# Optimization experiments

Measured on AMD Instinct MI355X. Metric: run time of the kernel, lower is better.

## Reference

```python
import jax, jax.numpy as jnp
import numpy as np

N_NODES = 50000
N_EDGES = 600000
N_COMM = 500
COMM_EDGES = 8000
NFEAT = 128
NHID = 128
NCLASS = 10
NLAYERS = 3
NHEADS = 8
EPS = 1e-5


def setup_inputs() -> dict:
    key = jax.random.key(0)
    ks = jax.random.split(key, 32)
    s = 0.05
    def rn(i, shape, scale=s):
        return (jax.random.normal(ks[i], shape, dtype=jnp.float32) * scale)
    return {
        "node_features": jax.random.normal(ks[0], (N_NODES, NFEAT), dtype=jnp.float32),
        "node_edge_index": jax.random.randint(ks[1], (2, N_EDGES), 0, N_NODES),
        "comm_features": jax.random.normal(ks[2], (N_COMM, NHID), dtype=jnp.float32),
        "comm_edge_index": jax.random.randint(ks[3], (2, COMM_EDGES), 0, N_COMM),
        "node_to_comm_map": jax.random.randint(ks[4], (N_NODES,), 0, N_COMM),
        # node-branch GCN params (nfeat == nhid so weights stack)
        "node_W": rn(5, (NLAYERS, NHID, NHID)),
        "node_b": rn(6, (NLAYERS, NHID)),
        "node_bn_g": 1.0 + rn(7, (NLAYERS, NHID)),
        "node_bn_b": rn(8, (NLAYERS, NHID)),
        # community-branch GCN params
        "comm_W": rn(9, (NLAYERS, NHID, NHID)),
        "comm_b": rn(10, (NLAYERS, NHID)),
        "comm_bn_g": 1.0 + rn(11, (NLAYERS, NHID)),
        "comm_bn_b": rn(12, (NLAYERS, NHID)),
        # MultiheadAttention params (torch layout: y = x @ W.T + b)
        "attn_in_w": rn(13, (3 * NHID, NHID)),
        "attn_in_b": rn(14, (3 * NHID,)),
        "attn_out_w": rn(15, (NHID, NHID)),
        "attn_out_b": rn(16, (NHID,)),
        # gate LayerNorm
        "ln_g": 1.0 + rn(17, (NHID,)),
        "ln_b": rn(18, (NHID,)),
        # classifier: Linear(128,64) -> BN -> ReLU -> Linear(64,10)
        "cls_W1": rn(19, (NHID, NHID // 2)),
        "cls_b1": rn(20, (NHID // 2,)),
        "cls_bn_g": 1.0 + rn(21, (NHID // 2,)),
        "cls_bn_b": rn(22, (NHID // 2,)),
        "cls_W2": rn(23, (NHID // 2, NCLASS)),
        "cls_b2": rn(24, (NCLASS,)),
    }


def _gcn_norm(edge_index, n):
    # PyG gcn_norm: add self-loops, symmetric D^-1/2 (A+I) D^-1/2
    loop = jnp.arange(n)
    src = jnp.concatenate([edge_index[0], loop])
    dst = jnp.concatenate([edge_index[1], loop])
    deg = jax.ops.segment_sum(jnp.ones(src.shape[0], jnp.float32), dst, num_segments=n)
    dinv = jnp.where(deg > 0, deg ** -0.5, 0.0)
    return src, dst, dinv[src] * dinv[dst]


def _gcn_stack(x, edge_index, Ws, bs, gs, betas):
    n = x.shape[0]
    src, dst, norm = _gcn_norm(edge_index, n)
    h = x
    for i in range(Ws.shape[0]):
        h_prev = h
        m = h @ Ws[i]  # linear commutes with normalized aggregation
        agg = jax.ops.segment_sum(m[src] * norm[:, None], dst, num_segments=n) + bs[i]
        mu = agg.mean(0)
        var = agg.var(0)  # biased, as torch BN training
        hb = (agg - mu) / jnp.sqrt(var + EPS) * gs[i] + betas[i]
        h = jax.nn.relu(hb)
        if i > 0:
            h = h + h_prev
    return h


def _mha(x, wi, bi, wo, bo):
    # x: [N, S=2, E]
    N, S, E = x.shape
    dh = E // NHEADS
    qkv = x @ wi.T + bi
    q, k, v = jnp.split(qkv, 3, axis=-1)
    q = q.reshape(N, S, NHEADS, dh)
    k = k.reshape(N, S, NHEADS, dh)
    v = v.reshape(N, S, NHEADS, dh)
    att = jnp.einsum('nqhd,nkhd->nhqk', q, k) / np.float32(np.sqrt(dh))
    att = jax.nn.softmax(att, axis=-1)
    o = jnp.einsum('nhqk,nkhd->nqhd', att, v).reshape(N, S, E)
    return o @ wo.T + bo


def reference(node_features, node_edge_index, comm_features, comm_edge_index,
              node_to_comm_map, node_W, node_b, node_bn_g, node_bn_b,
              comm_W, comm_b, comm_bn_g, comm_bn_b,
              attn_in_w, attn_in_b, attn_out_w, attn_out_b,
              ln_g, ln_b, cls_W1, cls_b1, cls_bn_g, cls_bn_b, cls_W2, cls_b2):
    h_node = _gcn_stack(node_features, node_edge_index, node_W, node_b, node_bn_g, node_bn_b)
    h_comm = _gcn_stack(comm_features, comm_edge_index, comm_W, comm_b, comm_bn_g, comm_bn_b)
    safe = jnp.clip(node_to_comm_map, 0, h_comm.shape[0] - 1)
    h_comm_exp = h_comm[safe]  # [N, nhid] cross-scale gather
    comb = jnp.stack([h_node, h_comm_exp], axis=1)  # [N, 2, nhid]
    attended = _mha(comb, attn_in_w, attn_in_b, attn_out_w, attn_out_b)
    x = attended.mean(axis=1) + h_node
    mu = x.mean(-1, keepdims=True)
    var = x.var(-1, keepdims=True)
    h_final = (x - mu) / jnp.sqrt(var + EPS) * ln_g + ln_b
    z = h_final @ cls_W1 + cls_b1
    zm = z.mean(0)
    zv = z.var(0)
    z = jax.nn.relu((z - zm) / jnp.sqrt(zv + EPS) * cls_bn_g + cls_bn_b)
    logits = z @ cls_W2 + cls_b2
    return jax.nn.log_softmax(logits, axis=-1)
```

## Files before the change

kernel.cpp:

```cpp
#include <hip/hip_runtime.h>
#include <hip/hip_bf16.h>
#include <cstdint>
#include <cstddef>


typedef __attribute__((ext_vector_type(8))) short bf16x8;
typedef __attribute__((ext_vector_type(4))) float f32x4;

#define EPSV 1e-5f

__device__ __forceinline__ float b2f(unsigned short u) {
    union { unsigned int i; float f; } x; x.i = ((unsigned int)u) << 16; return x.f;
}
__device__ __forceinline__ unsigned short f2b(float f) {
    union { float f; unsigned int i; } x; x.f = f;
    unsigned int i = x.i;
    return (unsigned short)((i + 0x7fffu + ((i >> 16) & 1u)) >> 16);
}

__global__ void prep_kernel(const float* __restrict__ node_W, const float* __restrict__ comm_W,
                            const float* __restrict__ cls_W1, const float* __restrict__ attn_in_w,
                            const float* __restrict__ attn_out_w, const float* __restrict__ comm_feat,
                            const float* __restrict__ node_feat,
                            unsigned short* __restrict__ WtN, unsigned short* __restrict__ WtC,
                            unsigned short* __restrict__ W1t, unsigned short* __restrict__ WinB,
                            unsigned short* __restrict__ WoutB, unsigned short* __restrict__ cfb,
                            unsigned short* __restrict__ nfb, int nC128, int nN128,
                            const int* __restrict__ ndst, int* __restrict__ cnt_n, int nE,
                            const int* __restrict__ cdst, int* __restrict__ cnt_c, int cE) {
    int idx = blockIdx.x * 256 + threadIdx.x;
    if (idx < 49152) {
        int l = idx >> 14, e = idx & 16383;
        int j = e & 7, lane = (e >> 3) & 63, kc = (e >> 9) & 3, t = e >> 11;
        int col = t * 16 + (lane & 15);
        int k = (lane >> 4) * 8 + kc * 32 + j;
        WtN[idx] = f2b(node_W[l * 16384 + k * 128 + col]); return;
    }
    idx -= 49152;
    if (idx < 49152) {
        int l = idx >> 14, e = idx & 16383;
        int j = e & 7, lane = (e >> 3) & 63, kc = (e >> 9) & 3, t = e >> 11;
        int col = t * 16 + (lane & 15);
        int k = (lane >> 4) * 8 + kc * 32 + j;
        WtC[idx] = f2b(comm_W[l * 16384 + k * 128 + col]); return;
    }
    idx -= 49152;
    if (idx < 8192) {
        int e = idx;
        int j = e & 7, lane = (e >> 3) & 63, kc = (e >> 9) & 3, t = e >> 11;
        int col = t * 16 + (lane & 15);
        int k = (lane >> 4) * 8 + kc * 32 + j;
        W1t[idx] = f2b(cls_W1[k * 64 + col]); return;
    }
    idx -= 8192;
    if (idx < 49152) {
        int e = idx;
        int j = e & 7, lane = (e >> 3) & 63, kc = (e >> 9) & 3, t = e >> 11;
        int col = t * 16 + (lane & 15);
        int k = (lane >> 4) * 8 + kc * 32 + j;
        WinB[idx] = f2b(attn_in_w[col * 128 + k]); return;
    }
    idx -= 49152;
    if (idx < 16384) {
        int e = idx;
        int j = e & 7, lane = (e >> 3) & 63, kc = (e >> 9) & 3, t = e >> 11;
        int col = t * 16 + (lane & 15);
        int k = (lane >> 4) * 8 + kc * 32 + j;
        WoutB[idx] = f2b(attn_out_w[col * 128 + k]); return;
    }
    idx -= 16384;
    if (idx < nC128) { cfb[idx] = f2b(comm_feat[idx]); return; }
    idx -= nC128;
    if (idx < nN128) { nfb[idx] = f2b(node_feat[idx]); return; }
    idx -= nN128;
    long eg = (long)idx * 4;
    if (eg < (long)nE + cE) {
        int dd[4]; int wh[4];
#pragma unroll
        for (int k = 0; k < 4; ++k) {
            long e = eg + k;
            if (e < nE) { dd[k] = ndst[e]; wh[k] = 0; }
            else if (e - nE < cE) { dd[k] = cdst[e - nE]; wh[k] = 1; }
            else wh[k] = -1;
        }
#pragma unroll
        for (int k = 0; k < 4; ++k) {
            if (wh[k] == 0) atomicAdd(&cnt_n[dd[k]], 1);
            else if (wh[k] == 1) atomicAdd(&cnt_c[dd[k]], 1);
        }
    }
}

__global__ void scan_block_dual(const int* __restrict__ cnt_n, int* __restrict__ rs_n,
                                int* __restrict__ bsum_n, int nN, int nbN,
                                const int* __restrict__ cnt_c, int* __restrict__ rs_c,
                                int* __restrict__ bsum_c, int nC,
                                float* __restrict__ di_n, float* __restrict__ di_c) {
    __shared__ int tmp[2048];
    int nbC = (nC + 1023) >> 10;
    int extra = (int)blockIdx.x - (nbN + nbC);
    if (extra >= 0) {
        int g = extra * 1024 + (int)threadIdx.x;
        if (g < nN) di_n[g] = rsqrtf((float)cnt_n[g] + 1.0f);
        else { int gc = g - nN; if (gc < nC) di_c[gc] = rsqrtf((float)cnt_c[gc] + 1.0f); }
        return;
    }
    const int* cnt; int* excl; int* bsum; int n, lb;
    if ((int)blockIdx.x < nbN) { cnt = cnt_n; excl = rs_n; bsum = bsum_n; n = nN; lb = blockIdx.x; }
    else { cnt = cnt_c; excl = rs_c; bsum = bsum_c; n = nC; lb = blockIdx.x - nbN; }
    int tid = threadIdx.x;
    int gid = lb * 1024 + tid;
    int v = (gid < n) ? ((cnt[gid] + 7) & ~7) : 0;
    int buf = 0;
    tmp[tid] = v;
    __syncthreads();
    for (int d = 1; d < 1024; d <<= 1) {
        int t = tmp[buf * 1024 + tid];
        int add = (tid >= d) ? tmp[buf * 1024 + tid - d] : 0;
        tmp[(1 - buf) * 1024 + tid] = t + add;
        buf = 1 - buf;
        __syncthreads();
    }
    int inc = tmp[buf * 1024 + tid];
    if (gid < n) excl[gid] = inc - v;
    if (tid == 1023) bsum[lb] = inc;
}

__global__ void scan_add_dual(int* __restrict__ rs_n, const int* __restrict__ bsum_n,
                              int* __restrict__ cur_n, int nN,
                              int* __restrict__ rs_c, const int* __restrict__ bsum_c,
                              int* __restrict__ cur_c, int nC) {
    int gid = blockIdx.x * 256 + threadIdx.x;
    if (gid < nN) {
        int lb = gid >> 10;
        int p = 0;
        for (int i = 0; i < lb; ++i) p += bsum_n[i];
        int v = rs_n[gid] + p;
        rs_n[gid] = v; cur_n[gid] = v;
    } else {
        int g = gid - nN;
        if (g < nC) {
            int lb = g >> 10;
            int p = 0;
            for (int i = 0; i < lb; ++i) p += bsum_c[i];
            int v = rs_c[g] + p;
            rs_c[g] = v; cur_c[g] = v;
        }
    }
}

__device__ __forceinline__ void gemm_wave_128(const unsigned short* __restrict__ A,
                                              const unsigned short* __restrict__ Bt,
                                              const float* __restrict__ di,
                                              unsigned short* __restrict__ D,
                                              int M, int m0, int lane) {
    int r = lane & 15, q = lane >> 4;
    int arow = m0 + r; if (arow >= M) arow = M - 1;
    const unsigned short* ap = A + (size_t)arow * 128 + q * 8;
    bf16x8 afrag[4];
#pragma unroll
    for (int kc = 0; kc < 4; ++kc)
        afrag[kc] = *(const bf16x8*)(const void*)(ap + kc * 32);
    float dsc[4];
#pragma unroll
    for (int t = 0; t < 4; ++t) {
        int row = m0 + q * 4 + t; if (row >= M) row = M - 1;
        dsc[t] = di[row];
    }
#pragma unroll
    for (int tt = 0; tt < 8; ++tt) {
        f32x4 acc = {0.f, 0.f, 0.f, 0.f};
#pragma unroll
        for (int kc = 0; kc < 4; ++kc) {
            bf16x8 bfrag = *(const bf16x8*)(const void*)(Bt + (((size_t)tt * 4 + kc) << 9) + lane * 8);
            acc = __builtin_amdgcn_mfma_f32_16x16x32_bf16(afrag[kc], bfrag, acc, 0, 0, 0);
        }
        int n0 = tt * 16;
#pragma unroll
        for (int t = 0; t < 4; ++t) {
            int row = m0 + q * 4 + t;
            if (row < M) D[(size_t)row * 128 + n0 + r] = f2b(acc[t] * dsc[t]);
        }
    }
}

__global__ __launch_bounds__(256) void gemm_fill_kernel(
    const unsigned short* __restrict__ A0, const unsigned short* __restrict__ Bt0,
    const float* __restrict__ di0, unsigned short* __restrict__ D0, int M0, int blocksA,
    const unsigned short* __restrict__ A1, const unsigned short* __restrict__ Bt1,
    const float* __restrict__ di1, unsigned short* __restrict__ D1, int M1, int blocksB,
    const int* __restrict__ ns, const int* __restrict__ ndst,
    int* __restrict__ cur_n, unsigned short* __restrict__ csrc_n, int nE,
    const int* __restrict__ cs, const int* __restrict__ cdst,
    int* __restrict__ cur_c, unsigned short* __restrict__ csrc_c, int cE) {
    int blk = blockIdx.x;
    if (blk < blocksA + blocksB) {
        const unsigned short *A, *Bt; const float* di; unsigned short* D; int M, lb;
        if (blk < blocksA) { A = A0; Bt = Bt0; di = di0; D = D0; M = M0; lb = blk; }
        else { A = A1; Bt = Bt1; di = di1; D = D1; M = M1; lb = blk - blocksA; }
        int m0 = (lb * 4 + (int)(threadIdx.x >> 6)) * 16;
        if (m0 >= M) return;
        gemm_wave_128(A, Bt, di, D, M, m0, threadIdx.x & 63);
        return;
    }
    long eg = ((long)(blk - blocksA - blocksB) * 256 + threadIdx.x) * 4;
    if (eg >= (long)nE + cE) return;
    int ss[4], pos[4], wh[4];
#pragma unroll
    for (int k = 0; k < 4; ++k) {
        long e = eg + k;
        if (e < nE) {
            ss[k] = ns[e]; int d = ndst[e];
            pos[k] = atomicAdd(&cur_n[d], 1); wh[k] = 0;
        } else if (e - nE < cE) {
            long ee = e - nE;
            ss[k] = cs[ee]; int d = cdst[ee];
            pos[k] = atomicAdd(&cur_c[d], 1); wh[k] = 1;
        } else wh[k] = -1;
    }
#pragma unroll
    for (int k = 0; k < 4; ++k) {
        if (wh[k] == 0)
            __builtin_nontemporal_store((unsigned short)(ss[k] + 1), csrc_n + pos[k]);
        else if (wh[k] == 1)
            __builtin_nontemporal_store((unsigned short)(ss[k] + 1), csrc_c + pos[k]);
    }
}

__global__ __launch_bounds__(256) void gather_dual(
    const unsigned short* __restrict__ m0, const int* __restrict__ rs0,
    const int* __restrict__ cnt0, const unsigned short* __restrict__ cs0,
    const float* __restrict__ di0, const float* __restrict__ b0,
    float* __restrict__ agg0, float* __restrict__ bins0, int n0, int blocksA,
    const unsigned short* __restrict__ m1, const int* __restrict__ rs1,
    const int* __restrict__ cnt1, const unsigned short* __restrict__ cs1,
    const float* __restrict__ di1, const float* __restrict__ b1,
    float* __restrict__ agg1, float* __restrict__ bins1, int n1) {
    __shared__ float lsum[4][128], lsq[4][128];
    int blk = blockIdx.x;
    const unsigned short* m; const int *rs, *cnt; const unsigned short* cs;
    const float *di, *bias;
    float *agg, *bins; int n, lb;
    if (blk < blocksA) { m = m0; rs = rs0; cnt = cnt0; cs = cs0; di = di0; bias = b0; agg = agg0; bins = bins0; n = n0; lb = blk; }
    else { m = m1; rs = rs1; cnt = cnt1; cs = cs1; di = di1; bias = b1; agg = agg1; bins = bins1; n = n1; lb = blk - blocksA; }
    int wib = threadIdx.x >> 6, lane = threadIdx.x & 63;
    int node = lb * 4 + wib;
    bool act = node < n;
    float a0 = 0.f, a1 = 0.f;
    if (act) {
        int start = rs[node];
        int end = start + ((cnt[node] + 7) & ~7);
        for (int i = start; i < end; i += 8) {
            int s[8]; unsigned int v[8];
#pragma unroll
            for (int j = 0; j < 8; ++j) s[j] = cs[i + j];
#pragma unroll
            for (int j = 0; j < 8; ++j) {
                int si = s[j] ? s[j] - 1 : node;
                v[j] = *(const unsigned int*)(m + (size_t)si * 128 + 2 * lane);
            }
#pragma unroll
            for (int j = 0; j < 8; ++j) {
                float wj = s[j] ? 1.f : 0.f;
                a0 += b2f((unsigned short)(v[j] & 0xffff)) * wj;
                a1 += b2f((unsigned short)(v[j] >> 16)) * wj;
            }
        }
        unsigned int v = *(const unsigned int*)(m + (size_t)node * 128 + 2 * lane);
        a0 += b2f((unsigned short)(v & 0xffff));
        a1 += b2f((unsigned short)(v >> 16));
        float d = di[node];
        a0 = a0 * d + bias[2 * lane];
        a1 = a1 * d + bias[2 * lane + 1];
        float2 o; o.x = a0; o.y = a1;
        ((float2*)(agg + (size_t)node * 128))[lane] = o;
    }
    lsum[wib][2 * lane] = a0;       lsum[wib][2 * lane + 1] = a1;
    lsq[wib][2 * lane] = a0 * a0;   lsq[wib][2 * lane + 1] = a1 * a1;
    __syncthreads();
    int t = threadIdx.x;
    int bb = (lb & 31) * 256;
    if (t < 128) {
        float v = lsum[0][t] + lsum[1][t] + lsum[2][t] + lsum[3][t];
        atomicAdd(&bins[bb + t], v);
    } else {
        int c = t - 128;
        float v = lsq[0][c] + lsq[1][c] + lsq[2][c] + lsq[3][c];
        atomicAdd(&bins[bb + 128 + c], v);
    }
}

__global__ __launch_bounds__(256) void applygemm_dual(
    const float* __restrict__ agg0, const float* __restrict__ bins0,
    const float* __restrict__ g0, const float* __restrict__ be0,
    unsigned short* __restrict__ hb0, const unsigned short* __restrict__ Bt0,
    const float* __restrict__ di0, unsigned short* __restrict__ D0,
    int n0, int blocksA, int useRes,
    const float* __restrict__ agg1, const float* __restrict__ bins1,
    const float* __restrict__ g1, const float* __restrict__ be1,
    unsigned short* __restrict__ hb1, const unsigned short* __restrict__ Bt1,
    const float* __restrict__ di1, unsigned short* __restrict__ D1, int n1) {
    __shared__ float sc[128], sh[128], bs[256];
    __shared__ unsigned short hrow_s[64 * 136];
    int blk = blockIdx.x;
    const float *agg, *bins, *g, *be, *di; unsigned short *hb, *D;
    const unsigned short* Bt; int n, lb;
    if (blk < blocksA) { agg = agg0; bins = bins0; g = g0; be = be0; hb = hb0; Bt = Bt0; di = di0; D = D0; n = n0; lb = blk; }
    else { agg = agg1; bins = bins1; g = g1; be = be1; hb = hb1; Bt = Bt1; di = di1; D = D1; n = n1; lb = blk - blocksA; }
    int t = threadIdx.x;
    {
        float a = 0.f;
#pragma unroll
        for (int b = 0; b < 32; ++b) a += bins[b * 256 + t];
        bs[t] = a;
    }
    __syncthreads();
    if (t < 128) {
        float inv = 1.f / (float)n;
        float mean = bs[t] * inv;
        float var = bs[128 + t] * inv - mean * mean;
        float rstd = rsqrtf(var + EPSV);
        float s = g[t] * rstd;
        sc[t] = s;
        sh[t] = be[t] - mean * s;
    }
    __syncthreads();
    int row0 = lb * 64;
#pragma unroll
    for (int it = 0; it < 8; ++it) {
        int base = row0 * 128 + it * 1024 + t * 4;
        if (base < n * 128) {
            float4 a = *(const float4*)(agg + base);
            ushort4 h = *(const ushort4*)(hb + base);
            int f = base & 127;
            float v0 = fmaxf(a.x * sc[f] + sh[f], 0.f);
            float v1 = fmaxf(a.y * sc[f + 1] + sh[f + 1], 0.f);
            float v2 = fmaxf(a.z * sc[f + 2] + sh[f + 2], 0.f);
            float v3 = fmaxf(a.w * sc[f + 3] + sh[f + 3], 0.f);
            if (useRes) { v0 += b2f(h.x); v1 += b2f(h.y); v2 += b2f(h.z); v3 += b2f(h.w); }
            ushort4 o; o.x = f2b(v0); o.y = f2b(v1); o.z = f2b(v2); o.w = f2b(v3);
            *(ushort4*)(hb + base) = o;
            int lr = (base >> 7) - row0;
            *(ushort4*)(hrow_s + lr * 136 + f) = o;
        }
    }
    __syncthreads();
    int lane = t & 63, w = t >> 6;
    int m0 = row0 + w * 16;
    if (m0 >= n) return;
    int r = lane & 15, q = lane >> 4;
    int arow = m0 + r; if (arow >= n) arow = n - 1;
    const unsigned short* ap = hrow_s + (arow - row0) * 136 + q * 8;
    bf16x8 afrag[4];
#pragma unroll
    for (int kc = 0; kc < 4; ++kc)
        afrag[kc] = *(const bf16x8*)(const void*)(ap + kc * 32);
    float dsc[4];
#pragma unroll
    for (int t4 = 0; t4 < 4; ++t4) {
        int row = m0 + q * 4 + t4; if (row >= n) row = n - 1;
        dsc[t4] = di[row];
    }
#pragma unroll
    for (int tt = 0; tt < 8; ++tt) {
        f32x4 acc = {0.f, 0.f, 0.f, 0.f};
#pragma unroll
        for (int kc = 0; kc < 4; ++kc) {
            bf16x8 bfrag = *(const bf16x8*)(const void*)(Bt + (((size_t)tt * 4 + kc) << 9) + lane * 8);
            acc = __builtin_amdgcn_mfma_f32_16x16x32_bf16(afrag[kc], bfrag, acc, 0, 0, 0);
        }
        int n0c = tt * 16;
#pragma unroll
        for (int t4 = 0; t4 < 4; ++t4) {
            int row = m0 + q * 4 + t4;
            if (row < n) D[(size_t)row * 128 + n0c + r] = f2b(acc[t4] * dsc[t4]);
        }
    }
}

__global__ __launch_bounds__(256) void apply_dual(
    const float* __restrict__ agg0, const float* __restrict__ bins0,
    const float* __restrict__ g0, const float* __restrict__ be0,
    unsigned short* __restrict__ hb0, int n0, int blocksA, int useRes,
    const float* __restrict__ agg1, const float* __restrict__ bins1,
    const float* __restrict__ g1, const float* __restrict__ be1,
    unsigned short* __restrict__ hb1, int n1,
    int doCq, const unsigned short* __restrict__ WinB,
    const float* __restrict__ binb, float* __restrict__ cqkv) {
    __shared__ float sc[128], sh[128], bs[256];
    __shared__ unsigned short crow_s[32 * 136];
    int blk = blockIdx.x;
    bool isComm = blk >= blocksA;
    const float *agg, *bins, *g, *be; unsigned short* hb; int n, lb;
    if (!isComm) { agg = agg0; bins = bins0; g = g0; be = be0; hb = hb0; n = n0; lb = blk; }
    else { agg = agg1; bins = bins1; g = g1; be = be1; hb = hb1; n = n1; lb = blk - blocksA; }
    int t = threadIdx.x;
    {
        float a = 0.f;
#pragma unroll
        for (int b = 0; b < 32; ++b) a += bins[b * 256 + t];
        bs[t] = a;
    }
    __syncthreads();
    if (t < 128) {
        float inv = 1.f / (float)n;
        float mean = bs[t] * inv;
        float var = bs[128 + t] * inv - mean * mean;
        float rstd = rsqrtf(var + EPSV);
        float s = g[t] * rstd;
        sc[t] = s;
        sh[t] = be[t] - mean * s;
    }
    __syncthreads();
    bool stage = doCq && isComm;
#pragma unroll
    for (int it = 0; it < 4; ++it) {
        int base = (lb * 4 + it) * 1024 + t * 4;
        if (base < n * 128) {
            float4 a = *(const float4*)(agg + base);
            ushort4 h = *(const ushort4*)(hb + base);
            int f = base & 127;
            float v0 = fmaxf(a.x * sc[f] + sh[f], 0.f);
            float v1 = fmaxf(a.y * sc[f + 1] + sh[f + 1], 0.f);
            float v2 = fmaxf(a.z * sc[f + 2] + sh[f + 2], 0.f);
            float v3 = fmaxf(a.w * sc[f + 3] + sh[f + 3], 0.f);
            if (useRes) { v0 += b2f(h.x); v1 += b2f(h.y); v2 += b2f(h.z); v3 += b2f(h.w); }
            ushort4 o; o.x = f2b(v0); o.y = f2b(v1); o.z = f2b(v2); o.w = f2b(v3);
            *(ushort4*)(hb + base) = o;
            if (stage) {
                int row = (base >> 7) - lb * 32;
                *(ushort4*)(crow_s + row * 136 + (base & 127)) = o;
            }
        }
    }
    if (stage) {
        __syncthreads();
        int lane = t & 63, w = t >> 6;
        int r = lane & 15, q = lane >> 4;
        int rg = w & 1;
        const unsigned short* ap = crow_s + (rg * 16 + r) * 136 + q * 8;
        bf16x8 afrag[4];
#pragma unroll
        for (int kc = 0; kc < 4; ++kc)
            afrag[kc] = *(const bf16x8*)(const void*)(ap + kc * 32);
        int t0 = (w >> 1) * 12;
        for (int tt = t0; tt < t0 + 12; ++tt) {
            f32x4 acc = {0.f, 0.f, 0.f, 0.f};
#pragma unroll
            for (int kc = 0; kc < 4; ++kc) {
                bf16x8 bfrag = *(const bf16x8*)(const void*)(WinB + (((size_t)tt * 4 + kc) << 9) + lane * 8);
                acc = __builtin_amdgcn_mfma_f32_16x16x32_bf16(afrag[kc], bfrag, acc, 0, 0, 0);
            }
            int n0c = tt * 16;
            float bv = binb[n0c + r];
#pragma unroll
            for (int t4 = 0; t4 < 4; ++t4) {
                int row = lb * 32 + rg * 16 + q * 4 + t4;
                if (row < n) cqkv[(size_t)row * 384 + n0c + r] = acc[t4] + bv;
            }
        }
    }
}

__global__ __launch_bounds__(256) void mha_fused_kernel(
    const unsigned short* __restrict__ hbn, const int* __restrict__ map,
    const float* __restrict__ cqkv,
    const unsigned short* __restrict__ WinB, const float* __restrict__ bin,
    const unsigned short* __restrict__ WoutB, const float* __restrict__ bout,
    const float* __restrict__ lng, const float* __restrict__ lnb,
    const unsigned short* __restrict__ W1t, const float* __restrict__ b1v,
    float* __restrict__ z, float* __restrict__ zbins, int nN, int nC) {
    __shared__ unsigned short obf_s[16 * 136];
    __shared__ float att_s[16 * 132];

    int b = blockIdx.x;
    int hg = threadIdx.x >> 6;
    int lane = threadIdx.x & 63;
    int r = lane & 15, q = lane >> 4;

    int arow = b * 16 + r; if (arow >= nN) arow = nN - 1;
    const unsigned short* ap = hbn + (size_t)arow * 128 + q * 8;
    bf16x8 afrag[4];
#pragma unroll
    for (int kc = 0; kc < 4; ++kc)
        afrag[kc] = *(const bf16x8*)(const void*)(ap + kc * 32);

    const float* cp[4];
#pragma unroll
    for (int t = 0; t < 4; ++t) {
        int nt = b * 16 + q * 4 + t; if (nt >= nN) nt = nN - 1;
        int c = map[nt]; c = c < 0 ? 0 : (c >= nC ? nC - 1 : c);
        cp[t] = cqkv + (size_t)c * 384;
    }

#pragma unroll
    for (int c = 0; c < 2; ++c) {
        int h = hg * 2 + c;
        f32x4 qa, ka, va;
#pragma unroll
        for (int p = 0; p < 3; ++p) {
            int tt = p * 8 + h;
            f32x4 acc = {0.f, 0.f, 0.f, 0.f};
#pragma unroll
            for (int kc = 0; kc < 4; ++kc) {
                bf16x8 bfrag = *(const bf16x8*)(const void*)(WinB + (((size_t)tt * 4 + kc) << 9) + lane * 8);
                acc = __builtin_amdgcn_mfma_f32_16x16x32_bf16(afrag[kc], bfrag, acc, 0, 0, 0);
            }
            float bv = bin[tt * 16 + r];
#pragma unroll
            for (int t = 0; t < 4; ++t) acc[t] += bv;
            if (p == 0) qa = acc; else if (p == 1) ka = acc; else va = acc;
        }
        float qc[4], kc_[4], vc[4];
#pragma unroll
        for (int t = 0; t < 4; ++t) {
            const float* cpt = cp[t] + h * 16 + r;
            qc[t] = cpt[0]; kc_[t] = cpt[128]; vc[t] = cpt[256];
        }
#pragma unroll
        for (int t = 0; t < 4; ++t) {
            float s00 = qa[t] * ka[t];
            float s01 = qa[t] * kc_[t];
            float s10 = qc[t] * ka[t];
            float s11 = qc[t] * kc_[t];
#pragma unroll
            for (int mku = 1; mku <= 8; mku <<= 1) {
                s00 += __shfl_xor(s00, mku); s01 += __shfl_xor(s01, mku);
                s10 += __shfl_xor(s10, mku); s11 += __shfl_xor(s11, mku);
            }
            s00 *= 0.25f; s01 *= 0.25f; s10 *= 0.25f; s11 *= 0.25f;
            float m0 = fmaxf(s00, s01), m1 = fmaxf(s10, s11);
            float e00 = __expf(s00 - m0), e01 = __expf(s01 - m0);
            float e10 = __expf(s10 - m1), e11 = __expf(s11 - m1);
            float i0 = 1.f / (e00 + e01), i1 = 1.f / (e10 + e11);
            float o0 = (e00 * va[t] + e01 * vc[t]) * i0;
            float o1 = (e10 * va[t] + e11 * vc[t]) * i1;
            obf_s[(q * 4 + t) * 136 + h * 16 + r] = f2b(0.5f * (o0 + o1));
        }
    }
    __syncthreads();

    bf16x8 ofrag[4];
#pragma unroll
    for (int kc = 0; kc < 4; ++kc)
        ofrag[kc] = *(const bf16x8*)(const void*)(obf_s + r * 136 + q * 8 + kc * 32);
#pragma unroll
    for (int c = 0; c < 2; ++c) {
        int tt = hg * 2 + c;
        f32x4 acc = {0.f, 0.f, 0.f, 0.f};
#pragma unroll
        for (int kc = 0; kc < 4; ++kc) {
            bf16x8 bfrag = *(const bf16x8*)(const void*)(WoutB + (((size_t)tt * 4 + kc) << 9) + lane * 8);
            acc = __builtin_amdgcn_mfma_f32_16x16x32_bf16(ofrag[kc], bfrag, acc, 0, 0, 0);
        }
        int n0 = tt * 16;
        float bv = bout[n0 + r];
#pragma unroll
        for (int t = 0; t < 4; ++t)
            att_s[(q * 4 + t) * 132 + n0 + r] = acc[t] + bv;
    }
    __syncthreads();
    unsigned short* hf_s = obf_s;

    {
        int nl = threadIdx.x >> 4;
        int j = threadIdx.x & 15;
        int gnode = b * 16 + nl;
        if (gnode >= nN) gnode = nN - 1;
        const unsigned short* hrow = hbn + (size_t)gnode * 128 + j * 8;
        ushort4 ha = *(const ushort4*)(hrow);
        ushort4 hbv = *(const ushort4*)(hrow + 4);
        float x[8]; float s = 0.f, s2 = 0.f;
        x[0] = att_s[nl * 132 + j * 8 + 0] + b2f(ha.x);
        x[1] = att_s[nl * 132 + j * 8 + 1] + b2f(ha.y);
        x[2] = att_s[nl * 132 + j * 8 + 2] + b2f(ha.z);
        x[3] = att_s[nl * 132 + j * 8 + 3] + b2f(ha.w);
        x[4] = att_s[nl * 132 + j * 8 + 4] + b2f(hbv.x);
        x[5] = att_s[nl * 132 + j * 8 + 5] + b2f(hbv.y);
        x[6] = att_s[nl * 132 + j * 8 + 6] + b2f(hbv.z);
        x[7] = att_s[nl * 132 + j * 8 + 7] + b2f(hbv.w);
#pragma unroll
        for (int i = 0; i < 8; ++i) { s += x[i]; s2 += x[i] * x[i]; }
        s += __shfl_xor(s, 1);  s2 += __shfl_xor(s2, 1);
        s += __shfl_xor(s, 2);  s2 += __shfl_xor(s2, 2);
        s += __shfl_xor(s, 4);  s2 += __shfl_xor(s2, 4);
        s += __shfl_xor(s, 8);  s2 += __shfl_xor(s2, 8);
        float mu = s * (1.f / 128.f);
        float var = s2 * (1.f / 128.f) - mu * mu;
        float rstd = rsqrtf(var + EPSV);
        ushort4 o1, o2;
        o1.x = f2b((x[0] - mu) * rstd * lng[j * 8 + 0] + lnb[j * 8 + 0]);
        o1.y = f2b((x[1] - mu) * rstd * lng[j * 8 + 1] + lnb[j * 8 + 1]);
        o1.z = f2b((x[2] - mu) * rstd * lng[j * 8 + 2] + lnb[j * 8 + 2]);
        o1.w = f2b((x[3] - mu) * rstd * lng[j * 8 + 3] + lnb[j * 8 + 3]);
        o2.x = f2b((x[4] - mu) * rstd * lng[j * 8 + 4] + lnb[j * 8 + 4]);
        o2.y = f2b((x[5] - mu) * rstd * lng[j * 8 + 5] + lnb[j * 8 + 5]);
        o2.z = f2b((x[6] - mu) * rstd * lng[j * 8 + 6] + lnb[j * 8 + 6]);
        o2.w = f2b((x[7] - mu) * rstd * lng[j * 8 + 7] + lnb[j * 8 + 7]);
        *(ushort4*)(hf_s + nl * 136 + j * 8) = o1;
        *(ushort4*)(hf_s + nl * 136 + j * 8 + 4) = o2;
    }
    __syncthreads();

    {
        bf16x8 hfrag[4];
#pragma unroll
        for (int kc = 0; kc < 4; ++kc)
            hfrag[kc] = *(const bf16x8*)(const void*)(hf_s + r * 136 + q * 8 + kc * 32);
        f32x4 acc = {0.f, 0.f, 0.f, 0.f};
#pragma unroll
        for (int kc = 0; kc < 4; ++kc) {
            bf16x8 bfrag = *(const bf16x8*)(const void*)(W1t + (((size_t)hg * 4 + kc) << 9) + lane * 8);
            acc = __builtin_amdgcn_mfma_f32_16x16x32_bf16(hfrag[kc], bfrag, acc, 0, 0, 0);
        }
        float bv = b1v[hg * 16 + r];
        float s = 0.f, s2 = 0.f;
#pragma unroll
        for (int t = 0; t < 4; ++t) {
            int row = b * 16 + q * 4 + t;
            if (row < nN) {
                float v = acc[t] + bv;
                z[(size_t)row * 64 + hg * 16 + r] = v;
                s += v; s2 += v * v;
            }
        }
        s += __shfl_xor(s, 16);  s2 += __shfl_xor(s2, 16);
        s += __shfl_xor(s, 32);  s2 += __shfl_xor(s2, 32);
        if (lane < 16) {
            int bb = (b & 31) * 128;
            atomicAdd(&zbins[bb + hg * 16 + r], s);
            atomicAdd(&zbins[bb + 64 + hg * 16 + r], s2);
        }
    }
}

__global__ __launch_bounds__(256) void final_kernel(const float* __restrict__ z,
                                                    const float* __restrict__ zbins,
                                                    const float* __restrict__ g,
                                                    const float* __restrict__ be,
                                                    const float* __restrict__ W2,
                                                    const float* __restrict__ b2v,
                                                    float* __restrict__ out, int nN) {
    __shared__ float zs[128];
    int t = threadIdx.x;
    if (t < 128) {
        float a = 0.f;
#pragma unroll
        for (int b = 0; b < 32; ++b) a += zbins[b * 128 + t];
        zs[t] = a;
    }
    __syncthreads();
    int lane = t & 63;
    float inv = 1.f / (float)nN;
    float mean = zs[lane] * inv;
    float var = zs[64 + lane] * inv - mean * mean;
    float sc = g[lane] * rsqrtf(var + EPSV);
    float sh = be[lane] - mean * sc;
    const float* wrow = W2 + lane * 10;
#pragma unroll
    for (int it = 0; it < 4; ++it) {
        int node = blockIdx.x * 16 + (t >> 6) * 4 + it;
        float v = 0.f;
        if (node < nN) v = fmaxf(z[(size_t)node * 64 + lane] * sc + sh, 0.f);
        float p[10];
#pragma unroll
        for (int c = 0; c < 10; ++c) p[c] = v * wrow[c];
#pragma unroll
        for (int off = 32; off >= 1; off >>= 1) {
#pragma unroll
            for (int c = 0; c < 10; ++c) p[c] += __shfl_xor(p[c], off);
        }
        if (node < nN) {
            float l[10], mx = -1e30f;
#pragma unroll
            for (int c = 0; c < 10; ++c) { l[c] = p[c] + b2v[c]; mx = fmaxf(mx, l[c]); }
            float se = 0.f;
#pragma unroll
            for (int c = 0; c < 10; ++c) se += expf(l[c] - mx);
            float lse = mx + logf(se);
            if (lane < 10) out[(size_t)node * 10 + lane] = l[lane] - lse;
        }
    }
}

static inline int cdiv(long a, long b) { return (int)((a + b - 1) / b); }

extern "C" void kernel_launch(void* const* d_in, const int* in_sizes, int n_in,
                              void* d_out, int out_size, void* d_ws, size_t ws_size,
                              hipStream_t stream) {
    const float* node_feat = (const float*)d_in[0];
    const int*   nedge     = (const int*)d_in[1];
    const float* comm_feat = (const float*)d_in[2];
    const int*   cedge     = (const int*)d_in[3];
    const int*   n2c       = (const int*)d_in[4];
    const float* node_W    = (const float*)d_in[5];
    const float* node_b    = (const float*)d_in[6];
    const float* node_g    = (const float*)d_in[7];
    const float* node_beta = (const float*)d_in[8];
    const float* comm_W    = (const float*)d_in[9];
    const float* comm_b    = (const float*)d_in[10];
    const float* comm_g    = (const float*)d_in[11];
    const float* comm_beta = (const float*)d_in[12];
    const float* attn_in_w = (const float*)d_in[13];
    const float* attn_in_b = (const float*)d_in[14];
    const float* attn_out_w= (const float*)d_in[15];
    const float* attn_out_b= (const float*)d_in[16];
    const float* ln_g      = (const float*)d_in[17];
    const float* ln_b      = (const float*)d_in[18];
    const float* cls_W1    = (const float*)d_in[19];
    const float* cls_b1    = (const float*)d_in[20];
    const float* cls_bn_g  = (const float*)d_in[21];
    const float* cls_bn_b  = (const float*)d_in[22];
    const float* cls_W2    = (const float*)d_in[23];
    const float* cls_b2    = (const float*)d_in[24];

    const int nN = in_sizes[0] / 128;
    const int nE = in_sizes[1] / 2;
    const int nC = in_sizes[2] / 128;
    const int cE = in_sizes[3] / 2;
    const int padE_n = nE + 8 * nN;
    const int padE_c = cE + 8 * nC;

    char* ws = (char*)d_ws;
    size_t off = 0;
    auto alloc = [&](size_t bytes) -> char* {
        char* p = ws + off;
        off = (off + bytes + 255) & ~(size_t)255;
        return p;
    };
    size_t zero_begin = off;
    int*   cnt_n  = (int*)alloc((size_t)nN * 4);
    int*   cur_n  = (int*)alloc((size_t)nN * 4);
    int*   cnt_c  = (int*)alloc((size_t)nC * 4);
    int*   cur_c  = (int*)alloc((size_t)nC * 4);
    float* bins_n = (float*)alloc((size_t)3 * 32 * 256 * 4);
    float* bins_c = (float*)alloc((size_t)3 * 32 * 256 * 4);
    float* zbins  = (float*)alloc((size_t)32 * 128 * 4);
    unsigned short* csrc_n = (unsigned short*)alloc((size_t)padE_n * 2);
    unsigned short* csrc_c = (unsigned short*)alloc((size_t)padE_c * 2);
    size_t zero_bytes = off - zero_begin;
    int*   rs_n   = (int*)alloc((size_t)(nN + 1) * 4);
    int*   bsum_n = (int*)alloc(256 * 4);
    float* dinv_n = (float*)alloc((size_t)nN * 4);
    int*   rs_c   = (int*)alloc((size_t)(nC + 1) * 4);
    int*   bsum_c = (int*)alloc(256 * 4);
    float* dinv_c = (float*)alloc((size_t)nC * 4);
    unsigned short* hb_n  = (unsigned short*)alloc((size_t)nN * 256);
    unsigned short* hb_c  = (unsigned short*)alloc((size_t)nC * 256);
    unsigned short* cfb   = (unsigned short*)alloc((size_t)nC * 256);
    unsigned short* m_cb  = (unsigned short*)alloc((size_t)nC * 256);
    float*          agg_c = (float*)alloc((size_t)nC * 512);
    float*          cqkv  = (float*)alloc((size_t)nC * 384 * 4);
    unsigned short* WtN  = (unsigned short*)alloc((size_t)3 * 16384 * 2);
    unsigned short* WtC  = (unsigned short*)alloc((size_t)3 * 16384 * 2);
    unsigned short* W1t  = (unsigned short*)alloc((size_t)64 * 128 * 2);
    unsigned short* WinB = (unsigned short*)alloc((size_t)384 * 128 * 2);
    unsigned short* WoutB= (unsigned short*)alloc((size_t)128 * 128 * 2);
    unsigned short* m_nb = (unsigned short*)alloc((size_t)nN * 256);
    float*          agg_n= (float*)alloc((size_t)nN * 512);
    unsigned short* nfb  = (unsigned short*)agg_n;
    float*          z    = agg_n;

    hipMemsetAsync(ws + zero_begin, 0, zero_bytes, stream);

    long prepN = 49152L * 3 + 8192 + 16384 + (long)nC * 128 + (long)nN * 128;
    long cntThreads = ((long)nE + cE + 3) / 4;
    long prepTotal = prepN + cntThreads;
    prep_kernel<<<cdiv(prepTotal, 256), 256, 0, stream>>>(
        node_W, comm_W, cls_W1, attn_in_w, attn_out_w, comm_feat, node_feat,
        WtN, WtC, W1t, WinB, WoutB, cfb, nfb, nC * 128, nN * 128,
        nedge + nE, cnt_n, nE, cedge + cE, cnt_c, cE);

    int nbN = cdiv(nN, 1024), nbC = cdiv(nC, 1024);
    int dinvB = cdiv((long)nN + nC, 1024);
    scan_block_dual<<<nbN + nbC + dinvB, 1024, 0, stream>>>(
        cnt_n, rs_n, bsum_n, nN, nbN, cnt_c, rs_c, bsum_c, nC, dinv_n, dinv_c);
    scan_add_dual<<<cdiv((long)nN + nC, 256), 256, 0, stream>>>(
        rs_n, bsum_n, cur_n, nN, rs_c, bsum_c, cur_c, nC);

    int gemmA = cdiv(nN, 64), gemmB = cdiv(nC, 64);
    int fillB = cdiv((long)nE + cE, 1024);
    int gatA = cdiv(nN, 4), gatB = cdiv(nC, 4);
    int appA = cdiv((long)nN * 128, 4096), appB = cdiv((long)nC * 128, 4096);

    gemm_fill_kernel<<<gemmA + gemmB + fillB, 256, 0, stream>>>(
        nfb, WtN, dinv_n, m_nb, nN, gemmA,
        cfb, WtC, dinv_c, m_cb, nC, gemmB,
        nedge, nedge + nE, cur_n, csrc_n, nE,
        cedge, cedge + cE, cur_c, csrc_c, cE);
    gather_dual<<<gatA + gatB, 256, 0, stream>>>(
        m_nb, rs_n, cnt_n, csrc_n, dinv_n, node_b, agg_n, bins_n, nN, gatA,
        m_cb, rs_c, cnt_c, csrc_c, dinv_c, comm_b, agg_c, bins_c, nC);
    applygemm_dual<<<gemmA + gemmB, 256, 0, stream>>>(
        agg_n, bins_n, node_g, node_beta, hb_n, WtN + 16384, dinv_n, m_nb, nN, gemmA, 0,
        agg_c, bins_c, comm_g, comm_beta, hb_c, WtC + 16384, dinv_c, m_cb, nC);
    gather_dual<<<gatA + gatB, 256, 0, stream>>>(
        m_nb, rs_n, cnt_n, csrc_n, dinv_n, node_b + 128, agg_n, bins_n + 32 * 256, nN, gatA,
        m_cb, rs_c, cnt_c, csrc_c, dinv_c, comm_b + 128, agg_c, bins_c + 32 * 256, nC);
    applygemm_dual<<<gemmA + gemmB, 256, 0, stream>>>(
        agg_n, bins_n + 32 * 256, node_g + 128, node_beta + 128, hb_n, WtN + 2 * 16384, dinv_n, m_nb, nN, gemmA, 1,
        agg_c, bins_c + 32 * 256, comm_g + 128, comm_beta + 128, hb_c, WtC + 2 * 16384, dinv_c, m_cb, nC);
    gather_dual<<<gatA + gatB, 256, 0, stream>>>(
        m_nb, rs_n, cnt_n, csrc_n, dinv_n, node_b + 256, agg_n, bins_n + 2 * 32 * 256, nN, gatA,
        m_cb, rs_c, cnt_c, csrc_c, dinv_c, comm_b + 256, agg_c, bins_c + 2 * 32 * 256, nC);
    apply_dual<<<appA + appB, 256, 0, stream>>>(
        agg_n, bins_n + 2 * 32 * 256, node_g + 256, node_beta + 256, hb_n, nN, appA, 1,
        agg_c, bins_c + 2 * 32 * 256, comm_g + 256, comm_beta + 256, hb_c, nC,
        1, WinB, attn_in_b, cqkv);

    mha_fused_kernel<<<cdiv(nN, 16), 256, 0, stream>>>(
        hb_n, n2c, cqkv, WinB, attn_in_b, WoutB, attn_out_b, ln_g, ln_b,
        W1t, cls_b1, z, zbins, nN, nC);

    final_kernel<<<cdiv(nN, 16), 256, 0, stream>>>(
        z, zbins, cls_bn_g, cls_bn_b, cls_W2, cls_b2, (float*)d_out, nN);
}
```

Measured before the change: 446.0 us.

## Fuse final node-layer BN/ReLU/residual apply into MHA kernel via shared memory

The last node-branch apply step (batch-norm from bin sums, ReLU, residual add, bf16 pack) moves into the MHA kernel, which builds each 16-node tile of hidden states in shared memory. This removes the write and re-read of the node hidden tensor and leaves apply_dual handling only community nodes. In exchange every MHA block re-reduces the 32 BN bins and redoes the scale/shift setup, and gains extra shared memory and barriers. z is moved to a different buffer so agg_n stays intact for the fused read.

```diff
diff --git a/kernel.cpp b/kernel.cpp
--- a/kernel.cpp
+++ b/kernel.cpp
@@ -463,23 +463,72 @@
 }
 
 __global__ __launch_bounds__(256) void mha_fused_kernel(
-    const unsigned short* __restrict__ hbn, const int* __restrict__ map,
+    const float* __restrict__ agg, const float* __restrict__ binsL2,
+    const float* __restrict__ gbn, const float* __restrict__ bebn,
+    const unsigned short* __restrict__ hbo, const int* __restrict__ map,
     const float* __restrict__ cqkv,
     const unsigned short* __restrict__ WinB, const float* __restrict__ bin,
     const unsigned short* __restrict__ WoutB, const float* __restrict__ bout,
     const float* __restrict__ lng, const float* __restrict__ lnb,
     const unsigned short* __restrict__ W1t, const float* __restrict__ b1v,
     float* __restrict__ z, float* __restrict__ zbins, int nN, int nC) {
+    __shared__ float bs[256];
+    __shared__ float sc_s[128], sh_s[128];
+    __shared__ unsigned short hb_s[16 * 136];
     __shared__ unsigned short obf_s[16 * 136];
     __shared__ float att_s[16 * 132];
 
     int b = blockIdx.x;
-    int hg = threadIdx.x >> 6;
-    int lane = threadIdx.x & 63;
+    int t = threadIdx.x;
+    int hg = t >> 6;
+    int lane = t & 63;
     int r = lane & 15, q = lane >> 4;
 
+    {
+        float a = 0.f;
+#pragma unroll
+        for (int b2 = 0; b2 < 32; ++b2) a += binsL2[b2 * 256 + t];
+        bs[t] = a;
+    }
+    __syncthreads();
+    if (t < 128) {
+        float inv = 1.f / (float)nN;
+        float mean = bs[t] * inv;
+        float var = bs[128 + t] * inv - mean * mean;
+        float rstd = rsqrtf(var + EPSV);
+        float s = gbn[t] * rstd;
+        sc_s[t] = s;
+        sh_s[t] = bebn[t] - mean * s;
+    }
+    __syncthreads();
+    {
+        int base = b * 2048 + t * 8;
+        if (base < nN * 128) {
+            float4 a1 = *(const float4*)(agg + base);
+            float4 a2 = *(const float4*)(agg + base + 4);
+            ushort4 h1 = *(const ushort4*)(hbo + base);
+            ushort4 h2 = *(const ushort4*)(hbo + base + 4);
+            int f = base & 127;
+            float v0 = fmaxf(a1.x * sc_s[f] + sh_s[f], 0.f) + b2f(h1.x);
+            float v1 = fmaxf(a1.y * sc_s[f + 1] + sh_s[f + 1], 0.f) + b2f(h1.y);
+            float v2 = fmaxf(a1.z * sc_s[f + 2] + sh_s[f + 2], 0.f) + b2f(h1.z);
+            float v3 = fmaxf(a1.w * sc_s[f + 3] + sh_s[f + 3], 0.f) + b2f(h1.w);
+            float v4 = fmaxf(a2.x * sc_s[f + 4] + sh_s[f + 4], 0.f) + b2f(h2.x);
+            float v5 = fmaxf(a2.y * sc_s[f + 5] + sh_s[f + 5], 0.f) + b2f(h2.y);
+            float v6 = fmaxf(a2.z * sc_s[f + 6] + sh_s[f + 6], 0.f) + b2f(h2.z);
+            float v7 = fmaxf(a2.w * sc_s[f + 7] + sh_s[f + 7], 0.f) + b2f(h2.w);
+            int lr = (base >> 7) - b * 16;
+            ushort4 o1, o2;
+            o1.x = f2b(v0); o1.y = f2b(v1); o1.z = f2b(v2); o1.w = f2b(v3);
+            o2.x = f2b(v4); o2.y = f2b(v5); o2.z = f2b(v6); o2.w = f2b(v7);
+            *(ushort4*)(hb_s + lr * 136 + f) = o1;
+            *(ushort4*)(hb_s + lr * 136 + f + 4) = o2;
+        }
+    }
+    __syncthreads();
+
     int arow = b * 16 + r; if (arow >= nN) arow = nN - 1;
-    const unsigned short* ap = hbn + (size_t)arow * 128 + q * 8;
+    const unsigned short* ap = hb_s + (arow - b * 16) * 136 + q * 8;
     bf16x8 afrag[4];
 #pragma unroll
     for (int kc = 0; kc < 4; ++kc)
@@ -487,10 +536,10 @@
 
     const float* cp[4];
 #pragma unroll
-    for (int t = 0; t < 4; ++t) {
-        int nt = b * 16 + q * 4 + t; if (nt >= nN) nt = nN - 1;
+    for (int tt4 = 0; tt4 < 4; ++tt4) {
+        int nt = b * 16 + q * 4 + tt4; if (nt >= nN) nt = nN - 1;
         int c = map[nt]; c = c < 0 ? 0 : (c >= nC ? nC - 1 : c);
-        cp[t] = cqkv + (size_t)c * 384;
+        cp[tt4] = cqkv + (size_t)c * 384;
     }
 
 #pragma unroll
@@ -508,21 +557,21 @@
             }
             float bv = bin[tt * 16 + r];
 #pragma unroll
-            for (int t = 0; t < 4; ++t) acc[t] += bv;
+            for (int t4 = 0; t4 < 4; ++t4) acc[t4] += bv;
             if (p == 0) qa = acc; else if (p == 1) ka = acc; else va = acc;
         }
         float qc[4], kc_[4], vc[4];
 #pragma unroll
-        for (int t = 0; t < 4; ++t) {
-            const float* cpt = cp[t] + h * 16 + r;
-            qc[t] = cpt[0]; kc_[t] = cpt[128]; vc[t] = cpt[256];
-        }
-#pragma unroll
-        for (int t = 0; t < 4; ++t) {
-            float s00 = qa[t] * ka[t];
-            float s01 = qa[t] * kc_[t];
-            float s10 = qc[t] * ka[t];
-            float s11 = qc[t] * kc_[t];
+        for (int t4 = 0; t4 < 4; ++t4) {
+            const float* cpt = cp[t4] + h * 16 + r;
+            qc[t4] = cpt[0]; kc_[t4] = cpt[128]; vc[t4] = cpt[256];
+        }
+#pragma unroll
+        for (int t4 = 0; t4 < 4; ++t4) {
+            float s00 = qa[t4] * ka[t4];
+            float s01 = qa[t4] * kc_[t4];
+            float s10 = qc[t4] * ka[t4];
+            float s11 = qc[t4] * kc_[t4];
 #pragma unroll
             for (int mku = 1; mku <= 8; mku <<= 1) {
                 s00 += __shfl_xor(s00, mku); s01 += __shfl_xor(s01, mku);
@@ -533,9 +582,9 @@
             float e00 = __expf(s00 - m0), e01 = __expf(s01 - m0);
             float e10 = __expf(s10 - m1), e11 = __expf(s11 - m1);
             float i0 = 1.f / (e00 + e01), i1 = 1.f / (e10 + e11);
-            float o0 = (e00 * va[t] + e01 * vc[t]) * i0;
-            float o1 = (e10 * va[t] + e11 * vc[t]) * i1;
-            obf_s[(q * 4 + t) * 136 + h * 16 + r] = f2b(0.5f * (o0 + o1));
+            float o0 = (e00 * va[t4] + e01 * vc[t4]) * i0;
+            float o1 = (e10 * va[t4] + e11 * vc[t4]) * i1;
+            obf_s[(q * 4 + t4) * 136 + h * 16 + r] = f2b(0.5f * (o0 + o1));
         }
     }
     __syncthreads();
@@ -556,18 +605,18 @@
         int n0 = tt * 16;
         float bv = bout[n0 + r];
 #pragma unroll
-        for (int t = 0; t < 4; ++t)
-            att_s[(q * 4 + t) * 132 + n0 + r] = acc[t] + bv;
+        for (int t4 = 0; t4 < 4; ++t4)
+            att_s[(q * 4 + t4) * 132 + n0 + r] = acc[t4] + bv;
     }
     __syncthreads();
     unsigned short* hf_s = obf_s;
 
     {
-        int nl = threadIdx.x >> 4;
-        int j = threadIdx.x & 15;
+        int nl = t >> 4;
+        int j = t & 15;
         int gnode = b * 16 + nl;
         if (gnode >= nN) gnode = nN - 1;
-        const unsigned short* hrow = hbn + (size_t)gnode * 128 + j * 8;
+        const unsigned short* hrow = hb_s + (gnode - b * 16) * 136 + j * 8;
         ushort4 ha = *(const ushort4*)(hrow);
         ushort4 hbv = *(const ushort4*)(hrow + 4);
         float x[8]; float s = 0.f, s2 = 0.f;
@@ -616,10 +665,10 @@
         float bv = b1v[hg * 16 + r];
         float s = 0.f, s2 = 0.f;
 #pragma unroll
-        for (int t = 0; t < 4; ++t) {
-            int row = b * 16 + q * 4 + t;
+        for (int t4 = 0; t4 < 4; ++t4) {
+            int row = b * 16 + q * 4 + t4;
             if (row < nN) {
-                float v = acc[t] + bv;
+                float v = acc[t4] + bv;
                 z[(size_t)row * 64 + hg * 16 + r] = v;
                 s += v; s2 += v * v;
             }
@@ -759,7 +808,7 @@
     unsigned short* m_nb = (unsigned short*)alloc((size_t)nN * 256);
     float*          agg_n= (float*)alloc((size_t)nN * 512);
     unsigned short* nfb  = (unsigned short*)agg_n;
-    float*          z    = agg_n;
+    float*          z    = (float*)m_nb;
 
     hipMemsetAsync(ws + zero_begin, 0, zero_bytes, stream);
 
@@ -781,7 +830,7 @@
     int gemmA = cdiv(nN, 64), gemmB = cdiv(nC, 64);
     int fillB = cdiv((long)nE + cE, 1024);
     int gatA = cdiv(nN, 4), gatB = cdiv(nC, 4);
-    int appA = cdiv((long)nN * 128, 4096), appB = cdiv((long)nC * 128, 4096);
+    int appB = cdiv((long)nC * 128, 4096);
 
     gemm_fill_kernel<<<gemmA + gemmB + fillB, 256, 0, stream>>>(
         nfb, WtN, dinv_n, m_nb, nN, gemmA,
@@ -803,12 +852,13 @@
     gather_dual<<<gatA + gatB, 256, 0, stream>>>(
         m_nb, rs_n, cnt_n, csrc_n, dinv_n, node_b + 256, agg_n, bins_n + 2 * 32 * 256, nN, gatA,
         m_cb, rs_c, cnt_c, csrc_c, dinv_c, comm_b + 256, agg_c, bins_c + 2 * 32 * 256, nC);
-    apply_dual<<<appA + appB, 256, 0, stream>>>(
-        agg_n, bins_n + 2 * 32 * 256, node_g + 256, node_beta + 256, hb_n, nN, appA, 1,
+    apply_dual<<<appB, 256, 0, stream>>>(
+        agg_n, bins_n + 2 * 32 * 256, node_g + 256, node_beta + 256, hb_n, nN, 0, 1,
         agg_c, bins_c + 2 * 32 * 256, comm_g + 256, comm_beta + 256, hb_c, nC,
         1, WinB, attn_in_b, cqkv);
 
     mha_fused_kernel<<<cdiv(nN, 16), 256, 0, stream>>>(
+        agg_n, bins_n + 2 * 32 * 256, node_g + 256, node_beta + 256,
         hb_n, n2c, cqkv, WinB, attn_in_b, WoutB, attn_out_b, ln_g, ln_b,
         W1t, cls_b1, z, zbins, nN, nC);
 
```

New measurement: 441.3 us. Within noise of the previous version (-1.1%).
